# Optimization experiments

Measured on AMD Instinct MI355X. Metric: run time of the kernel, lower is better.

The kernel has to match this reference:

```python
import jax, jax.numpy as jnp
import numpy as np

B, S, IN1, IN2, H = 1024, 200, 128, 128, 128

def setup_inputs() -> dict:
    key = jax.random.key(0)
    k = jax.random.split(key, 8)
    inp = jax.random.normal(k[0], (B, S, IN1), dtype=jnp.float32)
    z = jax.random.normal(k[1], (B, IN2), dtype=jnp.float32)
    mask = jax.random.randint(k[2], (B, S), 0, 2, dtype=jnp.int32)
    # learned params (PyTorch Linear: y = x @ W.T + b; store transposed for x @ W)
    W1 = jax.random.normal(k[3], (IN1, H), dtype=jnp.float32) / np.sqrt(IN1)
    W2 = jax.random.normal(k[4], (IN2, H), dtype=jnp.float32) / np.sqrt(IN2)
    b2 = jax.random.normal(k[5], (H,), dtype=jnp.float32) * 0.02
    V = jax.random.normal(k[6], (H, 1), dtype=jnp.float32) / np.sqrt(H)
    bV = jax.random.normal(k[7], (1,), dtype=jnp.float32) * 0.02
    return {"input": inp, "z": z, "mask": mask, "W1": W1, "W2": W2, "b2": b2, "V": V, "bV": bV}

def reference(input, z, mask, W1, W2, b2, V, bV):
    # w1h: [B,S,H]; w2h: [B,1,H]
    w1h = jnp.einsum('bsd,dh->bsh', input, W1)
    w2h = (z @ W2 + b2)[:, None, :]
    u = jnp.tanh(w1h + w2h)                      # [B,S,H]
    att = (jnp.einsum('bsh,h->bs', u, V[:, 0]) + bV[0])  # [B,S]
    att = jnp.where(mask == 0, jnp.float32(-1e10), att)
    att = jax.nn.softmax(att, axis=1)            # softmax over S
    out = jnp.einsum('bs,bsd->bd', att, input)   # weighted sum pooling
    return out
```

## Files before the change

kernel.cpp:

```cpp
#include <hip/hip_runtime.h>
#include <hip/hip_bf16.h>

constexpr int S_ = 200;
constexpr int SP = 208;

typedef __attribute__((ext_vector_type(8))) short short8_t;
typedef __attribute__((ext_vector_type(4))) float float4_t;

__device__ inline unsigned short f2bf(float f) {
  unsigned int u = __float_as_uint(f);
  u += 0x7FFFu + ((u >> 16) & 1u);
  return (unsigned short)(u >> 16);
}
__device__ inline unsigned int pk2(float x, float y) {
  return (unsigned int)f2bf(x) | ((unsigned int)f2bf(y) << 16);
}

__global__ __launch_bounds__(256) void prep_frag_kernel(
    const float* __restrict__ W1, short8_t* __restrict__ frag_out) {
  const int fid = blockIdx.x * 256 + threadIdx.x;
  const int lane = fid & 63, kk = (fid >> 6) & 3, nh = fid >> 8;
  const int c = lane & 15, kb = lane >> 4;
  const int h = nh * 16 + c;
  union { short8_t s8; unsigned int u[4]; } cv;
  #pragma unroll
  for (int jp = 0; jp < 4; ++jp) {
    const int k = kk * 32 + kb * 8 + jp * 2;
    cv.u[jp] = pk2(W1[k * 128 + h], W1[(k + 1) * 128 + h]);
  }
  frag_out[fid] = cv.s8;
}

__global__ __launch_bounds__(256, 4) void m2o_attn_kernel(
    const float* __restrict__ input, const float* __restrict__ z,
    const int* __restrict__ mask, const float* __restrict__ W2,
    const float* __restrict__ b2, const float* __restrict__ V,
    const float* __restrict__ bV, const short8_t* __restrict__ frag,
    float* __restrict__ out) {
  __shared__ short8_t frag_lds[2048];
  __shared__ float w2h_part[2][128];
  __shared__ float att_part[2][SP];
  __shared__ float att_w[SP];
  __shared__ float pool[2][128];
  __shared__ float redA[4], redB[4];

  const int t = threadIdx.x;
  const int b = blockIdx.x;
  const int lane = t & 63;
  const int wid = t >> 6;
  const int c = lane & 15;
  const int kb = lane >> 4;

  const float* inb = input + (size_t)b * (S_ * 128);

  #pragma unroll
  for (int i = 0; i < 8; ++i) frag_lds[t + i * 256] = frag[t + i * 256];

  const int maskv = (t < S_) ? mask[(size_t)b * S_ + t] : 0;
  const float bVv = bV[0];

  {
    const int h = t & 127, ph = t >> 7;
    const float* zb = z + (size_t)b * 128 + ph * 64;
    float acc = (ph == 0) ? b2[h] : 0.f;
    #pragma unroll 8
    for (int d = 0; d < 64; ++d) acc = fmaf(zb[d], W2[(ph * 64 + d) * 128 + h], acc);
    w2h_part[ph][h] = acc;
  }

  const int hh_i = wid & 1, hh = hh_i * 64;
  float vv[4];
  #pragma unroll
  for (int n = 0; n < 4; ++n) vv[n] = V[hh + n * 16 + c];

  __syncthreads();

  float w2v[4];
  #pragma unroll
  for (int n = 0; n < 4; ++n) {
    const int h = hh + n * 16 + c;
    w2v[n] = w2h_part[0][h] + w2h_part[1][h];
  }

  const int half = wid >> 1;
  const int mt0 = half * 7;
  const int nmt = half ? 6 : 7;

  float4 pa[4][2];
  {
    const int arow = mt0 * 16 + c;
    const int lrow = arow < S_ ? arow : (S_ - 1);
    const float* rp = inb + lrow * 128 + kb * 8;
    #pragma unroll
    for (int kk = 0; kk < 4; ++kk) {
      pa[kk][0] = *reinterpret_cast<const float4*>(rp + kk * 32);
      pa[kk][1] = *reinterpret_cast<const float4*>(rp + kk * 32 + 4);
    }
  }

  for (int i = 0; i < nmt; ++i) {
    const int mt = mt0 + i;
    short8_t a[4];
    #pragma unroll
    for (int kk = 0; kk < 4; ++kk) {
      union { short8_t s8; unsigned int u[4]; } cv;
      cv.u[0] = pk2(pa[kk][0].x, pa[kk][0].y);
      cv.u[1] = pk2(pa[kk][0].z, pa[kk][0].w);
      cv.u[2] = pk2(pa[kk][1].x, pa[kk][1].y);
      cv.u[3] = pk2(pa[kk][1].z, pa[kk][1].w);
      a[kk] = cv.s8;
    }
    if (i + 1 < nmt) {
      const int arow = (mt + 1) * 16 + c;
      const int lrow = arow < S_ ? arow : (S_ - 1);
      const float* rp = inb + lrow * 128 + kb * 8;
      #pragma unroll
      for (int kk = 0; kk < 4; ++kk) {
        pa[kk][0] = *reinterpret_cast<const float4*>(rp + kk * 32);
        pa[kk][1] = *reinterpret_cast<const float4*>(rp + kk * 32 + 4);
      }
    }
    float4_t acc[4] = {{0.f, 0.f, 0.f, 0.f}, {0.f, 0.f, 0.f, 0.f},
                       {0.f, 0.f, 0.f, 0.f}, {0.f, 0.f, 0.f, 0.f}};
    #pragma unroll
    for (int kk = 0; kk < 4; ++kk) {
      #pragma unroll
      for (int n = 0; n < 4; ++n)
        acc[n] = __builtin_amdgcn_mfma_f32_16x16x32_bf16(
            a[kk], frag_lds[((hh_i * 4 + n) * 4 + kk) * 64 + lane], acc[n], 0, 0, 0);
    }
    #pragma unroll
    for (int r = 0; r < 4; ++r) {
      const int row = mt * 16 + kb * 4 + r;
      float p = 0.f;
      #pragma unroll
      for (int n = 0; n < 4; ++n) {
        const float x = acc[n][r] + w2v[n];
        const float e = __expf(x + x);
        const float u = 1.f - __fdividef(2.f, e + 1.f);
        p = fmaf(u, vv[n], p);
      }
      p += __shfl_xor(p, 1);
      p += __shfl_xor(p, 2);
      p += __shfl_xor(p, 4);
      p += __shfl_xor(p, 8);
      if (c == 0 && row < S_) att_part[hh_i][row] = p;
    }
  }
  __syncthreads();

  float logit = -3.0e38f, ee = 0.f;
  if (t < S_) {
    logit = att_part[0][t] + att_part[1][t] + bVv;
    if (maskv == 0) logit = -1e10f;
  }
  {
    float m = logit;
    #pragma unroll
    for (int off = 32; off; off >>= 1) m = fmaxf(m, __shfl_xor(m, off));
    if (lane == 0) redA[wid] = m;
  }
  __syncthreads();
  {
    const float M = fmaxf(fmaxf(redA[0], redA[1]), fmaxf(redA[2], redA[3]));
    ee = (t < S_) ? __expf(logit - M) : 0.f;
    float sg = ee;
    #pragma unroll
    for (int off = 32; off; off >>= 1) sg += __shfl_xor(sg, off);
    if (lane == 0) redB[wid] = sg;
  }
  __syncthreads();
  {
    const float Ssum = redB[0] + redB[1] + redB[2] + redB[3];
    if (t < SP) att_w[t] = (t < S_) ? __fdividef(ee, Ssum) : 0.f;
  }
  __syncthreads();

  {
    const int d = t & 127, ph = t >> 7;
    const float* pp = inb + (size_t)(ph * 100) * 128 + d;
    float a0 = 0.f;
    #pragma unroll 4
    for (int s = 0; s < 100; ++s) a0 = fmaf(att_w[ph * 100 + s], pp[s * 128], a0);
    pool[ph][d] = a0;
  }
  __syncthreads();
  if (t < 128) out[(size_t)b * 128 + t] = pool[0][t] + pool[1][t];
}

extern "C" void kernel_launch(void* const* d_in, const int* in_sizes, int n_in,
                              void* d_out, int out_size, void* d_ws, size_t ws_size,
                              hipStream_t stream) {
  const float* input = (const float*)d_in[0];
  const float* z     = (const float*)d_in[1];
  const int*   mask  = (const int*)d_in[2];
  const float* W1    = (const float*)d_in[3];
  const float* W2    = (const float*)d_in[4];
  const float* b2    = (const float*)d_in[5];
  const float* V     = (const float*)d_in[6];
  const float* bV    = (const float*)d_in[7];
  float* out = (float*)d_out;

  short8_t* frag_ws = (short8_t*)d_ws;
  prep_frag_kernel<<<8, 256, 0, stream>>>(W1, frag_ws);
  m2o_attn_kernel<<<1024, 256, 0, stream>>>(input, z, mask, W2, b2, V, bV,
                                            frag_ws, out);
}
```

Measured before the change: 196.9 us.

## Split each batch's sequence across two blocks with flash-style softmax merge

Each batch row is now handled by two blocks covering 100 sequence positions each. Each block writes a partial pooled vector plus its local max and exp-sum, and a new merge kernel combines the halves with rescaled exponentials. The z@W2 projection moves into a prep kernel that writes w2h to workspace. The goal is more blocks and finer work units to raise occupancy and latency hiding. The cost is an extra kernel launch, workspace traffic for partials, and each block reloading the W1 fragments.

```diff
diff --git a/kernel.cpp b/kernel.cpp
--- a/kernel.cpp
+++ b/kernel.cpp
@@ -2,7 +2,6 @@
 #include <hip/hip_bf16.h>
 
 constexpr int S_ = 200;
-constexpr int SP = 208;
 
 typedef __attribute__((ext_vector_type(8))) short short8_t;
 typedef __attribute__((ext_vector_type(4))) float float4_t;
@@ -16,90 +15,82 @@
   return (unsigned int)f2bf(x) | ((unsigned int)f2bf(y) << 16);
 }
 
-__global__ __launch_bounds__(256) void prep_frag_kernel(
-    const float* __restrict__ W1, short8_t* __restrict__ frag_out) {
-  const int fid = blockIdx.x * 256 + threadIdx.x;
-  const int lane = fid & 63, kk = (fid >> 6) & 3, nh = fid >> 8;
-  const int c = lane & 15, kb = lane >> 4;
-  const int h = nh * 16 + c;
-  union { short8_t s8; unsigned int u[4]; } cv;
-  #pragma unroll
-  for (int jp = 0; jp < 4; ++jp) {
-    const int k = kk * 32 + kb * 8 + jp * 2;
-    cv.u[jp] = pk2(W1[k * 128 + h], W1[(k + 1) * 128 + h]);
-  }
-  frag_out[fid] = cv.s8;
-}
-
-__global__ __launch_bounds__(256, 4) void m2o_attn_kernel(
-    const float* __restrict__ input, const float* __restrict__ z,
-    const int* __restrict__ mask, const float* __restrict__ W2,
-    const float* __restrict__ b2, const float* __restrict__ V,
+__global__ __launch_bounds__(256) void prep_kernel(
+    const float* __restrict__ z, const float* __restrict__ W1,
+    const float* __restrict__ W2, const float* __restrict__ b2,
+    float* __restrict__ w2h_out, short8_t* __restrict__ frag_out) {
+  const int blk = blockIdx.x, t = threadIdx.x;
+  if (blk < 512) {
+    const int gid = blk * 256 + t;
+    const int b = gid >> 7, h = gid & 127;
+    const float* zb = z + (size_t)b * 128;
+    float acc = b2[h];
+    #pragma unroll 8
+    for (int d = 0; d < 128; ++d) acc = fmaf(zb[d], W2[d * 128 + h], acc);
+    w2h_out[gid] = acc;
+  } else {
+    const int fid = (blk - 512) * 256 + t;
+    const int lane = fid & 63, kk = (fid >> 6) & 3, nh = fid >> 8;
+    const int c = lane & 15, kb = lane >> 4;
+    const int h = nh * 16 + c;
+    union { short8_t s8; unsigned int u[4]; } cv;
+    #pragma unroll
+    for (int jp = 0; jp < 4; ++jp) {
+      const int k = kk * 32 + kb * 8 + jp * 2;
+      cv.u[jp] = pk2(W1[k * 128 + h], W1[(k + 1) * 128 + h]);
+    }
+    frag_out[fid] = cv.s8;
+  }
+}
+
+__global__ __launch_bounds__(256, 4) void logits_pool_kernel(
+    const float* __restrict__ input, const int* __restrict__ mask,
+    const float* __restrict__ w2h, const float* __restrict__ V,
     const float* __restrict__ bV, const short8_t* __restrict__ frag,
-    float* __restrict__ out) {
+    float* __restrict__ P_out, float* __restrict__ mz_out) {
   __shared__ short8_t frag_lds[2048];
-  __shared__ float w2h_part[2][128];
-  __shared__ float att_part[2][SP];
-  __shared__ float att_w[SP];
+  __shared__ float att_part[2][112];
+  __shared__ float att_w[112];
   __shared__ float pool[2][128];
   __shared__ float redA[4], redB[4];
 
   const int t = threadIdx.x;
-  const int b = blockIdx.x;
-  const int lane = t & 63;
-  const int wid = t >> 6;
-  const int c = lane & 15;
-  const int kb = lane >> 4;
-
+  const int b = blockIdx.x >> 1, half = blockIdx.x & 1;
+  const int lane = t & 63, wid = t >> 6;
+  const int c = lane & 15, kb = lane >> 4;
+  const int rq = wid >> 1, hh_i = wid & 1, hh = hh_i * 64;
+  const int rbase = half * 100;
   const float* inb = input + (size_t)b * (S_ * 128);
 
   #pragma unroll
   for (int i = 0; i < 8; ++i) frag_lds[t + i * 256] = frag[t + i * 256];
 
-  const int maskv = (t < S_) ? mask[(size_t)b * S_ + t] : 0;
+  const int maskv = (t < 100) ? mask[(size_t)b * S_ + rbase + t] : 0;
   const float bVv = bV[0];
 
-  {
-    const int h = t & 127, ph = t >> 7;
-    const float* zb = z + (size_t)b * 128 + ph * 64;
-    float acc = (ph == 0) ? b2[h] : 0.f;
-    #pragma unroll 8
-    for (int d = 0; d < 64; ++d) acc = fmaf(zb[d], W2[(ph * 64 + d) * 128 + h], acc);
-    w2h_part[ph][h] = acc;
-  }
-
-  const int hh_i = wid & 1, hh = hh_i * 64;
-  float vv[4];
-  #pragma unroll
-  for (int n = 0; n < 4; ++n) vv[n] = V[hh + n * 16 + c];
-
-  __syncthreads();
-
-  float w2v[4];
+  float w2v[4], vv[4];
   #pragma unroll
   for (int n = 0; n < 4; ++n) {
-    const int h = hh + n * 16 + c;
-    w2v[n] = w2h_part[0][h] + w2h_part[1][h];
-  }
-
-  const int half = wid >> 1;
-  const int mt0 = half * 7;
-  const int nmt = half ? 6 : 7;
-
+    w2v[n] = w2h[b * 128 + hh + n * 16 + c];
+    vv[n] = V[hh + n * 16 + c];
+  }
+
+  const int ntiles = rq ? 3 : 4;
   float4 pa[4][2];
   {
-    const int arow = mt0 * 16 + c;
+    const int arow = rbase + rq * 16 + c;
     const int lrow = arow < S_ ? arow : (S_ - 1);
-    const float* rp = inb + lrow * 128 + kb * 8;
+    const float* rp = input + (size_t)b * (S_ * 128) + lrow * 128 + kb * 8;
     #pragma unroll
     for (int kk = 0; kk < 4; ++kk) {
       pa[kk][0] = *reinterpret_cast<const float4*>(rp + kk * 32);
       pa[kk][1] = *reinterpret_cast<const float4*>(rp + kk * 32 + 4);
     }
   }
-
-  for (int i = 0; i < nmt; ++i) {
-    const int mt = mt0 + i;
+  __syncthreads();
+
+  for (int i = 0; i < ntiles; ++i) {
+    const int rt = rq + 2 * i;
     short8_t a[4];
     #pragma unroll
     for (int kk = 0; kk < 4; ++kk) {
@@ -110,8 +101,8 @@
       cv.u[3] = pk2(pa[kk][1].z, pa[kk][1].w);
       a[kk] = cv.s8;
     }
-    if (i + 1 < nmt) {
-      const int arow = (mt + 1) * 16 + c;
+    if (i + 1 < ntiles) {
+      const int arow = rbase + (rt + 2) * 16 + c;
       const int lrow = arow < S_ ? arow : (S_ - 1);
       const float* rp = inb + lrow * 128 + kb * 8;
       #pragma unroll
@@ -131,7 +122,7 @@
     }
     #pragma unroll
     for (int r = 0; r < 4; ++r) {
-      const int row = mt * 16 + kb * 4 + r;
+      const int rel = rt * 16 + kb * 4 + r;
       float p = 0.f;
       #pragma unroll
       for (int n = 0; n < 4; ++n) {
@@ -144,13 +135,13 @@
       p += __shfl_xor(p, 2);
       p += __shfl_xor(p, 4);
       p += __shfl_xor(p, 8);
-      if (c == 0 && row < S_) att_part[hh_i][row] = p;
-    }
-  }
-  __syncthreads();
-
-  float logit = -3.0e38f, ee = 0.f;
-  if (t < S_) {
+      if (c == 0) att_part[hh_i][rel] = p;
+    }
+  }
+  __syncthreads();
+
+  float logit = -3.0e38f;
+  if (t < 100) {
     logit = att_part[0][t] + att_part[1][t] + bVv;
     if (maskv == 0) logit = -1e10f;
   }
@@ -161,31 +152,48 @@
     if (lane == 0) redA[wid] = m;
   }
   __syncthreads();
-  {
-    const float M = fmaxf(fmaxf(redA[0], redA[1]), fmaxf(redA[2], redA[3]));
-    ee = (t < S_) ? __expf(logit - M) : 0.f;
+  const float M = fmaxf(fmaxf(redA[0], redA[1]), fmaxf(redA[2], redA[3]));
+  {
+    const float ee = (t < 100) ? __expf(logit - M) : 0.f;
     float sg = ee;
     #pragma unroll
     for (int off = 32; off; off >>= 1) sg += __shfl_xor(sg, off);
     if (lane == 0) redB[wid] = sg;
-  }
-  __syncthreads();
-  {
-    const float Ssum = redB[0] + redB[1] + redB[2] + redB[3];
-    if (t < SP) att_w[t] = (t < S_) ? __fdividef(ee, Ssum) : 0.f;
-  }
-  __syncthreads();
+    if (t < 100) att_w[t] = ee;
+  }
+  __syncthreads();
+  const float Z = redB[0] + redB[1] + redB[2] + redB[3];
 
   {
     const int d = t & 127, ph = t >> 7;
-    const float* pp = inb + (size_t)(ph * 100) * 128 + d;
+    const float* pp = inb + (size_t)(rbase + ph * 50) * 128 + d;
     float a0 = 0.f;
-    #pragma unroll 4
-    for (int s = 0; s < 100; ++s) a0 = fmaf(att_w[ph * 100 + s], pp[s * 128], a0);
+    #pragma unroll 5
+    for (int s = 0; s < 50; ++s) a0 = fmaf(att_w[ph * 50 + s], pp[(size_t)s * 128], a0);
     pool[ph][d] = a0;
   }
   __syncthreads();
-  if (t < 128) out[(size_t)b * 128 + t] = pool[0][t] + pool[1][t];
+  if (t < 128)
+    P_out[((size_t)b * 2 + half) * 128 + t] = pool[0][t] + pool[1][t];
+  if (t == 0) {
+    mz_out[((size_t)b * 2 + half) * 2 + 0] = M;
+    mz_out[((size_t)b * 2 + half) * 2 + 1] = Z;
+  }
+}
+
+__global__ __launch_bounds__(256) void merge_kernel(
+    const float* __restrict__ P, const float* __restrict__ mz,
+    float* __restrict__ out) {
+  const int gid = blockIdx.x * 256 + threadIdx.x;
+  const int b = gid >> 7, d = gid & 127;
+  const float m0 = mz[b * 4 + 0], z0 = mz[b * 4 + 1];
+  const float m1 = mz[b * 4 + 2], z1 = mz[b * 4 + 3];
+  const float M = fmaxf(m0, m1);
+  const float s0 = __expf(m0 - M), s1 = __expf(m1 - M);
+  const float denom = s0 * z0 + s1 * z1;
+  out[gid] = __fdividef(
+      fmaf(s0, P[(size_t)(b * 2) * 128 + d], s1 * P[(size_t)(b * 2 + 1) * 128 + d]),
+      denom);
 }
 
 extern "C" void kernel_launch(void* const* d_in, const int* in_sizes, int n_in,
@@ -201,8 +209,14 @@
   const float* bV    = (const float*)d_in[7];
   float* out = (float*)d_out;
 
-  short8_t* frag_ws = (short8_t*)d_ws;
-  prep_frag_kernel<<<8, 256, 0, stream>>>(W1, frag_ws);
-  m2o_attn_kernel<<<1024, 256, 0, stream>>>(input, z, mask, W2, b2, V, bV,
-                                            frag_ws, out);
-}
+  char* ws = (char*)d_ws;
+  short8_t* frag_ws = (short8_t*)ws;
+  float* w2h_ws = (float*)(ws + 32768);
+  float* P_ws   = (float*)(ws + 557056);
+  float* mz_ws  = (float*)(ws + 1605632);
+
+  prep_kernel<<<520, 256, 0, stream>>>(z, W1, W2, b2, w2h_ws, frag_ws);
+  logits_pool_kernel<<<2048, 256, 0, stream>>>(input, mask, w2h_ws, V, bV,
+                                               frag_ws, P_ws, mz_ws);
+  merge_kernel<<<512, 256, 0, stream>>>(P_ws, mz_ws, out);
+}
```

New measurement: 232.9 us. +18.3%, slower.
